# Kernel tuning notes

Hardware: AMD Instinct MI355X
Metric: run time of the kernel (lower is better)

The kernel has to match this reference:

```python
import jax, jax.numpy as jnp
import numpy as np


def _schedule(epoch):
    # Mirrors SPLoss._adjust_N_ratio_q_t (epoch is a static Python int)
    if epoch <= 25:
        return 0.7, 2
    elif epoch <= 75:
        return 0.8, 0
    elif epoch <= 95:
        return 0.9, 0
    else:
        return 1.0, 0


def setup_inputs() -> dict:
    key = jax.random.key(0)
    k1, k2 = jax.random.split(key)
    B, C = 32768, 1000
    output = jax.random.normal(k1, (B, C), dtype=jnp.float32)
    target = jax.random.randint(k2, (B,), 0, C, dtype=jnp.int64)
    return {"output": output, "target": target, "epoch": 10}


def reference(output, target, epoch):
    N_ratio, q_t = _schedule(epoch)
    B = output.shape[0]
    # fused cross-entropy: log-softmax + per-sample gather
    logp = jax.nn.log_softmax(output, axis=-1)            # [B, C]
    ce_loss = -jnp.take_along_axis(logp, target[:, None], axis=1)[:, 0]  # [B]
    # sort-based quantile threshold
    sorted_ce = jnp.sort(ce_loss)                          # ascending
    lambda_t = sorted_ce[int(B * N_ratio)]
    # power reweight v_t = (1 - ce/lambda)^(1/(q_t-1)), zero past threshold, cap at 10
    exponent = 1.0 / (q_t - 1)
    v_t = (1.0 - ce_loss / lambda_t) ** exponent
    v_t = jnp.where(ce_loss >= lambda_t, 0.0, v_t)
    v_t = jnp.where(v_t >= 10.0, 10.0, v_t)
    return (ce_loss * v_t).mean()
```

## Files before the change

### kernel.cpp

```cpp
#include <hip/hip_runtime.h>
#include <math.h>


__device__ __forceinline__ unsigned f2u(float f) {
    unsigned u = __float_as_uint(f);
    return (u & 0x80000000u) ? ~u : (u | 0x80000000u);
}
__device__ __forceinline__ float u2f(unsigned u) {
    unsigned b = (u & 0x80000000u) ? (u & 0x7FFFFFFFu) : ~u;
    return __uint_as_float(b);
}

#define CE_WPB 4

__global__ __launch_bounds__(256) void ce_kernel(
        const float* __restrict__ x, const int* __restrict__ tgt,
        unsigned* __restrict__ ceu, int B, int C)
{
    const int lane = threadIdx.x & 63;
    const int wave = threadIdx.x >> 6;
    const int row  = blockIdx.x * CE_WPB + wave;
    if (row >= B) return;

    const float* rp = x + (size_t)row * C;
    const int C4 = C >> 2;
    const float4* p4 = (const float4*)rp;

    const float NEG = -INFINITY;
    float4 v0 = make_float4(NEG, NEG, NEG, NEG), v1 = v0, v2 = v0, v3 = v0;
    if (lane       < C4) v0 = p4[lane];
    if (lane +  64 < C4) v1 = p4[lane + 64];
    if (lane + 128 < C4) v2 = p4[lane + 128];
    if (lane + 192 < C4) v3 = p4[lane + 192];
    const float tv = rp[tgt[row]];

    float m = fmaxf(fmaxf(fmaxf(v0.x, v0.y), fmaxf(v0.z, v0.w)),
                    fmaxf(fmaxf(v1.x, v1.y), fmaxf(v1.z, v1.w)));
    m = fmaxf(m, fmaxf(fmaxf(v2.x, v2.y), fmaxf(v2.z, v2.w)));
    m = fmaxf(m, fmaxf(fmaxf(v3.x, v3.y), fmaxf(v3.z, v3.w)));
    for (int off = 32; off > 0; off >>= 1)
        m = fmaxf(m, __shfl_xor(m, off, 64));

    float s = __expf(v0.x - m) + __expf(v0.y - m) + __expf(v0.z - m) + __expf(v0.w - m)
            + __expf(v1.x - m) + __expf(v1.y - m) + __expf(v1.z - m) + __expf(v1.w - m)
            + __expf(v2.x - m) + __expf(v2.y - m) + __expf(v2.z - m) + __expf(v2.w - m)
            + __expf(v3.x - m) + __expf(v3.y - m) + __expf(v3.z - m) + __expf(v3.w - m);
    for (int off = 32; off > 0; off >>= 1)
        s += __shfl_xor(s, off, 64);

    if (lane == 0)
        ceu[row] = f2u((m + __logf(s)) - tv);
}

#define K2_T 1024
__global__ __launch_bounds__(K2_T) void select_kernel(
        const unsigned* __restrict__ ceu, const int* __restrict__ epoch_p,
        float* __restrict__ out, int B)
{
    __shared__ unsigned sv[32768];
    __shared__ unsigned sh[256];
    __shared__ unsigned s_prefix, s_k;
    __shared__ float    s_wsum[K2_T / 64];

    const int tid  = threadIdx.x;
    const int lane = tid & 63;
    const int wave = tid >> 6;

    const uint4* c4 = (const uint4*)ceu;
    const int n4 = B >> 2;
    for (int i = tid; i < n4; i += K2_T) ((uint4*)sv)[i] = c4[i];

    const int e = epoch_p[0];
    double nr; int qt;
    if (e <= 25)      { nr = 0.7; qt = 2; }
    else if (e <= 75) { nr = 0.8; qt = 0; }
    else if (e <= 95) { nr = 0.9; qt = 0; }
    else              { nr = 1.0; qt = 0; }
    const bool inv = (qt != 2);
    if (tid == 0) {
        long long kk = (long long)((double)B * nr);
        if (kk > (long long)B - 1) kk = (long long)B - 1;
        s_prefix = 0u;
        s_k = (unsigned)kk;
    }
    __syncthreads();

    for (int p = 0; p < 4; ++p) {
        if (tid < 256) sh[tid] = 0u;
        __syncthreads();
        const int shift = 24 - 8 * p;
        const unsigned hm   = p ? (0xFFFFFFFFu << (shift + 8)) : 0u;
        const unsigned pref = s_prefix;
        for (int j = tid; j < B; j += K2_T) {
            unsigned u = sv[j];
            if ((u & hm) == (pref & hm))
                atomicAdd(&sh[(u >> shift) & 255u], 1u);
        }
        __syncthreads();
        if (wave == 0) {
            unsigned c0 = sh[4 * lane], c1 = sh[4 * lane + 1];
            unsigned c2 = sh[4 * lane + 2], c3 = sh[4 * lane + 3];
            unsigned cw = c0 + c1 + c2 + c3;
            unsigned incl = cw;
            for (int off = 1; off < 64; off <<= 1) {
                unsigned t = __shfl_up(incl, off, 64);
                if (lane >= off) incl += t;
            }
            unsigned excl = incl - cw;
            unsigned kr = s_k;
            unsigned long long bm = __ballot(excl <= kr && kr < excl + cw);
            int L = __ffsll(bm) - 1;
            if (lane == L) {
                unsigned rem = kr - excl;
                int b; unsigned cum;
                if      (rem < c0)           { b = 0; cum = 0; }
                else if (rem < c0 + c1)      { b = 1; cum = c0; }
                else if (rem < c0 + c1 + c2) { b = 2; cum = c0 + c1; }
                else                         { b = 3; cum = c0 + c1 + c2; }
                s_k = rem - cum;
                s_prefix = pref | ((unsigned)(4 * lane + b) << shift);
            }
        }
        __syncthreads();
    }

    const float lam = u2f(s_prefix);
    float part = 0.0f;
    for (int j = tid; j < B; j += K2_T) {
        float c = u2f(sv[j]);
        float base = 1.0f - c / lam;
        float v = inv ? (1.0f / base) : base;
        if (c >= lam)       v = 0.0f;
        else if (v >= 10.f) v = 10.0f;
        part += c * v;
    }
    for (int off = 32; off > 0; off >>= 1) part += __shfl_xor(part, off, 64);
    if (lane == 0) s_wsum[wave] = part;
    __syncthreads();
    if (tid == 0) {
        float tot = 0.0f;
        for (int i = 0; i < K2_T / 64; ++i) tot += s_wsum[i];
        out[0] = tot / (float)B;
    }
}

extern "C" void kernel_launch(void* const* d_in, const int* in_sizes, int n_in,
                              void* d_out, int out_size, void* d_ws, size_t ws_size,
                              hipStream_t stream)
{
    const float* x     = (const float*)d_in[0];
    const int*   tgt   = (const int*)d_in[1];
    const int*   epoch = (const int*)d_in[2];
    int B = in_sizes[1];
    int C = in_sizes[0] / B;

    unsigned* ceu = (unsigned*)d_ws;

    int ceBlocks = (B + CE_WPB - 1) / CE_WPB;
    ce_kernel<<<ceBlocks, 256, 0, stream>>>(x, tgt, ceu, B, C);
    select_kernel<<<1, K2_T, 0, stream>>>(ceu, epoch, (float*)d_out, B);
}
```

Baseline: 227.0 us.

## Offload first radix-select histogram pass to a multi-block kernel

Adds a 16-block histogram kernel that builds the top-byte histogram of the CE keys in global memory. The single-block select kernel then reads it and only runs the remaining three radix passes, so less serial work sits in one workgroup. The global histogram is zeroed at the start of the CE kernel, and the target gather is hoisted ahead of the row loads. The cost is an extra kernel launch and global atomics.

```diff
diff --git a/kernel.cpp b/kernel.cpp
--- a/kernel.cpp
+++ b/kernel.cpp
@@ -15,24 +15,27 @@
 
 __global__ __launch_bounds__(256) void ce_kernel(
         const float* __restrict__ x, const int* __restrict__ tgt,
-        unsigned* __restrict__ ceu, int B, int C)
-{
+        unsigned* __restrict__ ceu, unsigned* __restrict__ ghist, int B, int C)
+{
+    if (blockIdx.x == 0 && threadIdx.x < 256) ghist[threadIdx.x] = 0u;
+
     const int lane = threadIdx.x & 63;
     const int wave = threadIdx.x >> 6;
     const int row  = blockIdx.x * CE_WPB + wave;
     if (row >= B) return;
 
     const float* rp = x + (size_t)row * C;
+    const int t = tgt[row];
+    const float tv = rp[t];
+
     const int C4 = C >> 2;
     const float4* p4 = (const float4*)rp;
-
     const float NEG = -INFINITY;
     float4 v0 = make_float4(NEG, NEG, NEG, NEG), v1 = v0, v2 = v0, v3 = v0;
     if (lane       < C4) v0 = p4[lane];
     if (lane +  64 < C4) v1 = p4[lane + 64];
     if (lane + 128 < C4) v2 = p4[lane + 128];
     if (lane + 192 < C4) v3 = p4[lane + 192];
-    const float tv = rp[tgt[row]];
 
     float m = fmaxf(fmaxf(fmaxf(v0.x, v0.y), fmaxf(v0.z, v0.w)),
                     fmaxf(fmaxf(v1.x, v1.y), fmaxf(v1.z, v1.w)));
@@ -52,10 +55,39 @@
         ceu[row] = f2u((m + __logf(s)) - tv);
 }
 
+__global__ __launch_bounds__(512) void hist0_kernel(
+        const unsigned* __restrict__ ceu, unsigned* __restrict__ ghist, int B)
+{
+    __shared__ unsigned wh[8][256];
+    const int tid  = threadIdx.x;
+    const int wave = tid >> 6;
+
+    #pragma unroll
+    for (int j = 0; j < 4; ++j) wh[(tid * 4 + j) >> 8][(tid * 4 + j) & 255] = 0u;
+    __syncthreads();
+
+    const int i = blockIdx.x * 512 + tid;
+    if (i * 4 < B) {
+        uint4 u = ((const uint4*)ceu)[i];
+        atomicAdd(&wh[wave][u.x >> 24], 1u);
+        atomicAdd(&wh[wave][u.y >> 24], 1u);
+        atomicAdd(&wh[wave][u.z >> 24], 1u);
+        atomicAdd(&wh[wave][u.w >> 24], 1u);
+    }
+    __syncthreads();
+
+    if (tid < 256) {
+        unsigned s = 0;
+        #pragma unroll
+        for (int w = 0; w < 8; ++w) s += wh[w][tid];
+        if (s) atomicAdd(&ghist[tid], s);
+    }
+}
+
 #define K2_T 1024
 __global__ __launch_bounds__(K2_T) void select_kernel(
-        const unsigned* __restrict__ ceu, const int* __restrict__ epoch_p,
-        float* __restrict__ out, int B)
+        const unsigned* __restrict__ ceu, const unsigned* __restrict__ ghist,
+        const int* __restrict__ epoch_p, float* __restrict__ out, int B)
 {
     __shared__ unsigned sv[32768];
     __shared__ unsigned sh[256];
@@ -66,9 +98,8 @@
     const int lane = tid & 63;
     const int wave = tid >> 6;
 
-    const uint4* c4 = (const uint4*)ceu;
     const int n4 = B >> 2;
-    for (int i = tid; i < n4; i += K2_T) ((uint4*)sv)[i] = c4[i];
+    for (int i = tid; i < n4; i += K2_T) ((uint4*)sv)[i] = ((const uint4*)ceu)[i];
 
     const int e = epoch_p[0];
     double nr; int qt;
@@ -77,19 +108,40 @@
     else if (e <= 95) { nr = 0.9; qt = 0; }
     else              { nr = 1.0; qt = 0; }
     const bool inv = (qt != 2);
-    if (tid == 0) {
+
+    if (wave == 0) {
         long long kk = (long long)((double)B * nr);
         if (kk > (long long)B - 1) kk = (long long)B - 1;
-        s_prefix = 0u;
-        s_k = (unsigned)kk;
-    }
-    __syncthreads();
-
-    for (int p = 0; p < 4; ++p) {
+        uint4 g = ((const uint4*)ghist)[lane];
+        unsigned c0 = g.x, c1 = g.y, c2 = g.z, c3 = g.w;
+        unsigned cw = c0 + c1 + c2 + c3;
+        unsigned incl = cw;
+        for (int off = 1; off < 64; off <<= 1) {
+            unsigned t = __shfl_up(incl, off, 64);
+            if (lane >= off) incl += t;
+        }
+        unsigned excl = incl - cw;
+        unsigned kr = (unsigned)kk;
+        unsigned long long bm = __ballot(excl <= kr && kr < excl + cw);
+        int L = __ffsll(bm) - 1;
+        if (lane == L) {
+            unsigned rem = kr - excl;
+            int b; unsigned cum;
+            if      (rem < c0)           { b = 0; cum = 0; }
+            else if (rem < c0 + c1)      { b = 1; cum = c0; }
+            else if (rem < c0 + c1 + c2) { b = 2; cum = c0 + c1; }
+            else                         { b = 3; cum = c0 + c1 + c2; }
+            s_k = rem - cum;
+            s_prefix = (unsigned)(4 * L + b) << 24;
+        }
+    }
+    __syncthreads();
+
+    for (int p = 1; p < 4; ++p) {
         if (tid < 256) sh[tid] = 0u;
         __syncthreads();
         const int shift = 24 - 8 * p;
-        const unsigned hm   = p ? (0xFFFFFFFFu << (shift + 8)) : 0u;
+        const unsigned hm   = 0xFFFFFFFFu << (shift + 8);
         const unsigned pref = s_prefix;
         for (int j = tid; j < B; j += K2_T) {
             unsigned u = sv[j];
@@ -154,9 +206,11 @@
     int B = in_sizes[1];
     int C = in_sizes[0] / B;
 
-    unsigned* ceu = (unsigned*)d_ws;
+    unsigned* ceu   = (unsigned*)d_ws;
+    unsigned* ghist = ceu + B;
 
     int ceBlocks = (B + CE_WPB - 1) / CE_WPB;
-    ce_kernel<<<ceBlocks, 256, 0, stream>>>(x, tgt, ceu, B, C);
-    select_kernel<<<1, K2_T, 0, stream>>>(ceu, epoch, (float*)d_out, B);
-}
+    ce_kernel<<<ceBlocks, 256, 0, stream>>>(x, tgt, ceu, ghist, B, C);
+    hist0_kernel<<<16, 512, 0, stream>>>(ceu, ghist, B);
+    select_kernel<<<1, K2_T, 0, stream>>>(ceu, ghist, epoch, (float*)d_out, B);
+}
```

Measured after the change: 212.2 us. 6.5% less time.
